# Kernel optimization log

Measured on AMD Instinct MI355X. Metric: run time of the kernel, lower is better.

## Reference

```python
import jax, jax.numpy as jnp
import numpy as np

NUM_HEADS = 32
NUM_KV_HEADS = 8
HEAD_DIM = 128
ROPE_THETA = 1000000.0
SCALING = HEAD_DIM ** -0.5


def apply_rope_neox(x, positions):
    # x: [T, H, D], positions: [T] int
    half = HEAD_DIM // 2
    inv_freq = 1.0 / (ROPE_THETA ** (jnp.arange(0, half, dtype=jnp.float32) / half))
    freqs = positions.astype(jnp.float32)[:, None] * inv_freq[None, :]  # [T, D/2]
    cos = jnp.cos(freqs)[:, None, :]  # [T, 1, D/2]
    sin = jnp.sin(freqs)[:, None, :]
    x1, x2 = x[..., :half], x[..., half:]
    return jnp.concatenate([x1 * cos - x2 * sin, x2 * cos + x1 * sin], axis=-1)


def setup_inputs() -> dict:
    key = jax.random.key(0)
    k1, k2, k3 = jax.random.split(key, 3)
    T, H = 2048, 4096
    positions = jnp.arange(T, dtype=jnp.int32)
    hidden_states = jax.random.normal(k1, (T, H), dtype=jnp.float32)
    Wqkv = jax.random.normal(k2, (H, 6144), dtype=jnp.float32) * 0.02
    Wo = jax.random.normal(k3, (H, H), dtype=jnp.float32) * 0.02
    return {"positions": positions, "hidden_states": hidden_states, "Wqkv": Wqkv, "Wo": Wo}


def reference(positions, hidden_states, Wqkv, Wo):
    T = hidden_states.shape[0]
    q_size = NUM_HEADS * HEAD_DIM
    kv_size = NUM_KV_HEADS * HEAD_DIM
    qkv = hidden_states @ Wqkv  # [T, 6144]
    q = qkv[:, :q_size].reshape(T, NUM_HEADS, HEAD_DIM)
    k = qkv[:, q_size:q_size + kv_size].reshape(T, NUM_KV_HEADS, HEAD_DIM)
    v = qkv[:, q_size + kv_size:].reshape(T, NUM_KV_HEADS, HEAD_DIM)
    q = apply_rope_neox(q, positions)
    k = apply_rope_neox(k, positions)
    # GQA: repeat kv heads to match query heads
    rep = NUM_HEADS // NUM_KV_HEADS
    k = jnp.repeat(k, rep, axis=1)  # [T, H, D]
    v = jnp.repeat(v, rep, axis=1)
    scores = jnp.einsum('thd,shd->hts', q, k) * SCALING  # [H, T, T]
    causal = jnp.tril(jnp.ones((T, T), dtype=bool))
    scores = jnp.where(causal[None], scores, jnp.finfo(scores.dtype).min)
    attn = jax.nn.softmax(scores, axis=-1)
    out = jnp.einsum('hts,shd->thd', attn, v).reshape(T, NUM_HEADS * HEAD_DIM)
    return out @ Wo
```

## Files before the change

### kernel.cpp

```cpp
#include <hip/hip_runtime.h>
#include <math.h>

#define T_TOK 2048
#define HDIM  4096
#define QKVN  6144
#define NHEADS 32
#define HD    128
#define KV_OFF 4096
#define V_OFF  5120
#define SCALE 0.08838834764831843f

typedef __attribute__((ext_vector_type(8))) short short8;
typedef __attribute__((ext_vector_type(4))) float f32x4;
typedef __attribute__((ext_vector_type(16))) float f32x16;

__device__ __forceinline__ ushort f2bf(float f) {
    union { float f; unsigned u; } v; v.f = f;
    unsigned r = v.u + 0x7FFFu + ((v.u >> 16) & 1u);
    return (ushort)(r >> 16);
}

template <int N_, int K_>
__global__ __launch_bounds__(256) void gemm_bf16(const ushort* __restrict__ A,
                                                 const ushort* __restrict__ B,
                                                 float* __restrict__ C) {
    __shared__ ushort As[128 * 32];
    __shared__ ushort Bs[128 * 32];

    const int tid = threadIdx.x;
    const int w = tid >> 6;
    const int l = tid & 63;
    const int bm = blockIdx.y * 128;
    const int bn = blockIdx.x * 128;
    const int wm = (w & 1) * 64;
    const int wn = (w >> 1) * 64;

    f32x4 acc[4][4];
#pragma unroll
    for (int i = 0; i < 4; i++)
#pragma unroll
        for (int j = 0; j < 4; j++) acc[i][j] = (f32x4){0.f, 0.f, 0.f, 0.f};

    const ushort* ag = A + (size_t)(bm + (tid >> 2)) * K_ + (tid & 3) * 8;
    const ushort* bg = B + (size_t)(bn + (tid >> 2)) * K_ + (tid & 3) * 8;

    auto ldsA = (__attribute__((address_space(3))) char*)As;
    auto ldsB = (__attribute__((address_space(3))) char*)Bs;
    const int wb = w * 1024;

    for (int k0 = 0; k0 < K_; k0 += 32) {
        __syncthreads();
        __builtin_amdgcn_global_load_lds(
            (const __attribute__((address_space(1))) void*)ag,
            (__attribute__((address_space(3))) void*)(ldsA + wb), 16, 0, 0);
        __builtin_amdgcn_global_load_lds(
            (const __attribute__((address_space(1))) void*)(ag + (size_t)64 * K_),
            (__attribute__((address_space(3))) void*)(ldsA + 4096 + wb), 16, 0, 0);
        __builtin_amdgcn_global_load_lds(
            (const __attribute__((address_space(1))) void*)bg,
            (__attribute__((address_space(3))) void*)(ldsB + wb), 16, 0, 0);
        __builtin_amdgcn_global_load_lds(
            (const __attribute__((address_space(1))) void*)(bg + (size_t)64 * K_),
            (__attribute__((address_space(3))) void*)(ldsB + 4096 + wb), 16, 0, 0);
        ag += 32;
        bg += 32;
        __syncthreads();

        short8 af[4], bfr[4];
#pragma unroll
        for (int i = 0; i < 4; i++)
            af[i] = *(const short8*)&As[(wm + 16 * i + (l & 15)) * 32 + (l >> 4) * 8];
#pragma unroll
        for (int j = 0; j < 4; j++)
            bfr[j] = *(const short8*)&Bs[(wn + 16 * j + (l & 15)) * 32 + (l >> 4) * 8];
#pragma unroll
        for (int i = 0; i < 4; i++)
#pragma unroll
            for (int j = 0; j < 4; j++)
                acc[i][j] = __builtin_amdgcn_mfma_f32_16x16x32_bf16(af[i], bfr[j], acc[i][j], 0, 0, 0);
    }

    const int cn = bn + wn + (l & 15);
    const int rm = bm + wm + (l >> 4) * 4;
#pragma unroll
    for (int i = 0; i < 4; i++)
#pragma unroll
        for (int j = 0; j < 4; j++)
#pragma unroll
            for (int r = 0; r < 4; r++)
                C[(size_t)(rm + 16 * i + r) * N_ + cn + 16 * j] = acc[i][j][r];
}

__global__ __launch_bounds__(256) void cast_bf16(const float* __restrict__ in,
                                                 ushort* __restrict__ outp) {
    const int i = (blockIdx.x * 256 + threadIdx.x) * 4;
    float4 v = *(const float4*)(in + i);
    ushort4 o = {f2bf(v.x), f2bf(v.y), f2bf(v.z), f2bf(v.w)};
    *(ushort4*)(outp + i) = o;
}

template <int K_, int N_>
__global__ __launch_bounds__(256) void transpose_cast(const float* __restrict__ W,
                                                      ushort* __restrict__ WT) {
    __shared__ float T[32 * 65];
    const int k0 = blockIdx.y * 32;
    const int n0 = blockIdx.x * 64;
    const int x = threadIdx.x & 63;
    const int y = threadIdx.x >> 6;
#pragma unroll
    for (int p = 0; p < 8; p++) {
        const int kk = p * 4 + y;
        T[kk * 65 + x] = W[(size_t)(k0 + kk) * N_ + n0 + x];
    }
    __syncthreads();
#pragma unroll
    for (int q = 0; q < 4; q++) {
        const int nl = q * 16 + (threadIdx.x >> 4);
        const int k2 = (threadIdx.x & 15) * 2;
        ushort2 o = {f2bf(T[k2 * 65 + nl]), f2bf(T[(k2 + 1) * 65 + nl])};
        *(ushort2*)&WT[(size_t)(n0 + nl) * K_ + k0 + k2] = o;
    }
}

__global__ __launch_bounds__(256) void rope_cast(const int* __restrict__ pos,
                                                 const float* __restrict__ qkv,
                                                 ushort* __restrict__ qkB) {
    const int t = blockIdx.x;
    const int slot = blockIdx.y * 4 + (threadIdx.x >> 6);
    const int d = threadIdx.x & 63;
    const float p = (float)pos[t];
    const float invf = exp2f(-(float)d * (19.931568569324174f / 64.0f));
    const float f = p * invf;
    const float c = cosf(f), s = sinf(f);
    const float sc = (slot < 32) ? SCALE : 1.0f;
    const float* base = qkv + (size_t)t * QKVN + slot * HD;
    ushort* ob = qkB + (size_t)t * QKVN + slot * HD;
    const float x1 = base[d];
    const float x2 = base[d + 64];
    ob[d]      = f2bf((x1 * c - x2 * s) * sc);
    ob[d + 64] = f2bf((x2 * c + x1 * s) * sc);
}

__global__ __launch_bounds__(256) void vt_cast(const float* __restrict__ qkv,
                                               ushort* __restrict__ Vt) {
    __shared__ float tile[32][33];
    const int t0 = blockIdx.x * 32;
    const int c0 = blockIdx.y * 32;
    const int tx = threadIdx.x & 31;
    const int ty = threadIdx.x >> 5;
#pragma unroll
    for (int i = 0; i < 4; i++) {
        const int tt = ty + 8 * i;
        tile[tt][tx] = qkv[(size_t)(t0 + tt) * QKVN + V_OFF + c0 + tx];
    }
    __syncthreads();
#pragma unroll
    for (int i = 0; i < 4; i++) {
        const int dd = ty + 8 * i;
        Vt[(size_t)(c0 + dd) * 2048 + t0 + tx] = f2bf(tile[tx][dd]);
    }
}

__global__ __launch_bounds__(256, 2) void flash_attn_mfma(
        const ushort* __restrict__ qkB,
        const ushort* __restrict__ Vt,
        ushort* __restrict__ attnB) {
    __shared__ ushort Kf[8 * 512];
    __shared__ ushort Vf[8 * 512];

    const int b = blockIdx.x;
    const int half = b >> 8;
    const int rest = b & 255;
    const int h = rest >> 3;
    const int q8 = rest & 7;
    const int qi = half ? (15 - q8) : q8;
    const int kvh = h >> 2;

    const int tid = threadIdx.x;
    const int w = tid >> 6;
    const int l = tid & 63;
    const int l31 = l & 31;
    const int hf = l >> 5;

    const int qg = qi * 128 + w * 32 + l31;

    short8 qf[8];
    {
        const ushort* qrow = qkB + (size_t)qg * QKVN + h * HD + hf * 8;
#pragma unroll
        for (int kt = 0; kt < 8; kt++)
            qf[kt] = *(const short8*)(qrow + kt * 16);
    }

    f32x16 O[4];
#pragma unroll
    for (int dt = 0; dt < 4; dt++)
#pragma unroll
        for (int r = 0; r < 16; r++) O[dt][r] = 0.f;
    float mcur = -INFINITY, lcur = 0.f;

    const ushort* kbase = qkB + (size_t)l31 * QKVN + KV_OFF + kvh * HD + (2 * w) * 16 + hf * 8;
    const ushort* vbase = Vt + ((size_t)(kvh * 128 + w * 32 + l31)) * 2048 + hf * 8;

    auto ldsK = (__attribute__((address_space(3))) char*)Kf;
    auto ldsV = (__attribute__((address_space(3))) char*)Vf;

    const int nst = 4 * qi + 4;
    const int mylast = 4 * qi + w;

    for (int st = 0; st < nst; st++) {
        __syncthreads();
        {
            const ushort* kg = kbase + (size_t)st * 32 * QKVN;
            __builtin_amdgcn_global_load_lds(
                (const __attribute__((address_space(1))) void*)kg,
                (__attribute__((address_space(3))) void*)(ldsK + (2 * w) * 1024), 16, 0, 0);
            __builtin_amdgcn_global_load_lds(
                (const __attribute__((address_space(1))) void*)(kg + 16),
                (__attribute__((address_space(3))) void*)(ldsK + (2 * w + 1) * 1024), 16, 0, 0);
            const ushort* vg = vbase + st * 32;
            __builtin_amdgcn_global_load_lds(
                (const __attribute__((address_space(1))) void*)vg,
                (__attribute__((address_space(3))) void*)(ldsV + (2 * w) * 1024), 16, 0, 0);
            __builtin_amdgcn_global_load_lds(
                (const __attribute__((address_space(1))) void*)(vg + 16),
                (__attribute__((address_space(3))) void*)(ldsV + (2 * w + 1) * 1024), 16, 0, 0);
        }
        __syncthreads();

        if (st <= mylast) {
            f32x16 S;
#pragma unroll
            for (int r = 0; r < 16; r++) S[r] = 0.f;
#pragma unroll
            for (int kt = 0; kt < 8; kt++) {
                short8 afK = *(const short8*)&Kf[kt * 512 + l * 8];
                S = __builtin_amdgcn_mfma_f32_32x32x16_bf16(afK, qf[kt], S, 0, 0, 0);
            }

            float p[16];
#pragma unroll
            for (int r = 0; r < 16; r++) p[r] = S[r];
            if (st == mylast) {
                const int sb = st * 32 + 4 * hf;
#pragma unroll
                for (int r = 0; r < 16; r++) {
                    const int sg = sb + (r & 3) + 8 * (r >> 2);
                    if (sg > qg) p[r] = -INFINITY;
                }
            }
            float rmax = p[0];
#pragma unroll
            for (int r = 1; r < 16; r++) rmax = fmaxf(rmax, p[r]);
            rmax = fmaxf(rmax, __shfl_xor(rmax, 32));
            const float mnew = fmaxf(mcur, rmax);
            const float alpha = __expf(mcur - mnew);
            float rsum = 0.f;
#pragma unroll
            for (int r = 0; r < 16; r++) {
                p[r] = __expf(p[r] - mnew);
                rsum += p[r];
            }
            rsum += __shfl_xor(rsum, 32);
            lcur = lcur * alpha + rsum;
            mcur = mnew;

#pragma unroll
            for (int dt = 0; dt < 4; dt++)
#pragma unroll
                for (int r = 0; r < 16; r++) O[dt][r] *= alpha;

            unsigned pk[8], rk[8];
#pragma unroll
            for (int g = 0; g < 4; g++) {
                pk[2 * g]     = (unsigned)f2bf(p[4 * g])     | ((unsigned)f2bf(p[4 * g + 1]) << 16);
                pk[2 * g + 1] = (unsigned)f2bf(p[4 * g + 2]) | ((unsigned)f2bf(p[4 * g + 3]) << 16);
            }
#pragma unroll
            for (int i = 0; i < 8; i++) rk[i] = (unsigned)__shfl_xor((int)pk[i], 32);

            short8 Pf[2];
#pragma unroll
            for (int kt2 = 0; kt2 < 2; kt2++) {
                const int g = 2 * kt2 + hf;
                union { unsigned u[4]; short8 s; } cvt;
                cvt.u[0] = hf ? rk[2 * g]     : pk[2 * g];
                cvt.u[1] = hf ? rk[2 * g + 1] : pk[2 * g + 1];
                cvt.u[2] = hf ? pk[2 * g]     : rk[2 * g];
                cvt.u[3] = hf ? pk[2 * g + 1] : rk[2 * g + 1];
                Pf[kt2] = cvt.s;
            }

#pragma unroll
            for (int dt = 0; dt < 4; dt++)
#pragma unroll
                for (int kt2 = 0; kt2 < 2; kt2++) {
                    short8 afV = *(const short8*)&Vf[(dt * 2 + kt2) * 512 + l * 8];
                    O[dt] = __builtin_amdgcn_mfma_f32_32x32x16_bf16(afV, Pf[kt2], O[dt], 0, 0, 0);
                }
        }
    }

    const float inv = 1.0f / lcur;
    ushort* orow = attnB + (size_t)qg * HDIM + h * HD + 4 * hf;
#pragma unroll
    for (int dt = 0; dt < 4; dt++)
#pragma unroll
        for (int rg = 0; rg < 4; rg++) {
            ushort4 o;
            o.x = f2bf(O[dt][4 * rg + 0] * inv);
            o.y = f2bf(O[dt][4 * rg + 1] * inv);
            o.z = f2bf(O[dt][4 * rg + 2] * inv);
            o.w = f2bf(O[dt][4 * rg + 3] * inv);
            *(ushort4*)(orow + dt * 32 + 8 * rg) = o;
        }
}

__global__ __launch_bounds__(256) void rope_kernel(const int* __restrict__ pos,
                                                   float* __restrict__ qkv) {
    const int t = blockIdx.x;
    const int head = blockIdx.y * 4 + (threadIdx.x >> 6);
    const int d = threadIdx.x & 63;
    const float p = (float)pos[t];
    const float invf = exp2f(-(float)d * (19.931568569324174f / 64.0f));
    const float f = p * invf;
    const float c = cosf(f), s = sinf(f);
    float* base = qkv + (size_t)t * QKVN + head * HD;
    const float x1 = base[d];
    const float x2 = base[d + 64];
    base[d]      = x1 * c - x2 * s;
    base[d + 64] = x2 * c + x1 * s;
}

#define DOT4(acc, a, b) acc += (a).x*(b).x + (a).y*(b).y + (a).z*(b).z + (a).w*(b).w
#define FMA4(o, p, v) { (o).x += (p)*(v).x; (o).y += (p)*(v).y; (o).z += (p)*(v).z; (o).w += (p)*(v).w; }

__global__ __launch_bounds__(256, 2) void flash_attn_f32(const float* __restrict__ qkv,
                                                         float* __restrict__ out) {
    __shared__ float Qs[64 * 132];
    __shared__ float KVs[32 * 132];
    __shared__ float Ps[64 * 34];
    const int b = blockIdx.x;
    const int half = (b >> 9) & 1;
    const int rest = b & 511;
    const int h = rest >> 4;
    const int qlo = rest & 15;
    const int qi = half ? (31 - qlo) : qlo;
    const int kvh = h >> 2;
    const int tid = threadIdx.x;
    const int tx = tid & 7;
    const int ty = tid >> 3;
    {
        const float* qbase = qkv + (size_t)(qi * 64) * QKVN + h * HD;
#pragma unroll
        for (int r = 0; r < 8; r++) {
            int idx = r * 256 + tid;
            int qrow = idx >> 5;
            int d = (idx & 31) * 4;
            float4 v = *(const float4*)(qbase + (size_t)qrow * QKVN + d);
            v.x *= SCALE; v.y *= SCALE; v.z *= SCALE; v.w *= SCALE;
            *(float4*)(Qs + qrow * 132 + d) = v;
        }
    }
    float m[2], lsm[2];
    float4 O[2][4];
#pragma unroll
    for (int i = 0; i < 2; i++) {
        m[i] = -INFINITY; lsm[i] = 0.f;
#pragma unroll
        for (int jj = 0; jj < 4; jj++) O[i][jj] = make_float4(0.f, 0.f, 0.f, 0.f);
    }
    const float* kbase = qkv + KV_OFF + kvh * HD;
    const float* vbase = qkv + V_OFF + kvh * HD;
    const int qg0 = qi * 64 + ty;
    const int nst = 2 * qi + 2;
    for (int st = 0; st < nst; st++) {
        __syncthreads();
#pragma unroll
        for (int r = 0; r < 4; r++) {
            int idx = r * 256 + tid;
            int srow = idx >> 5;
            int d = (idx & 31) * 4;
            *(float4*)(KVs + srow * 132 + d) =
                *(const float4*)(kbase + (size_t)(st * 32 + srow) * QKVN + d);
        }
        __syncthreads();
        float S[2][4];
#pragma unroll
        for (int i = 0; i < 2; i++)
#pragma unroll
            for (int j = 0; j < 4; j++) S[i][j] = 0.f;
#pragma unroll 4
        for (int kk = 0; kk < HD; kk += 4) {
            float4 q0 = *(const float4*)(Qs + ty * 132 + kk);
            float4 q1 = *(const float4*)(Qs + (ty + 32) * 132 + kk);
            float4 k0 = *(const float4*)(KVs + tx * 132 + kk);
            float4 k1 = *(const float4*)(KVs + (tx + 8) * 132 + kk);
            float4 k2 = *(const float4*)(KVs + (tx + 16) * 132 + kk);
            float4 k3 = *(const float4*)(KVs + (tx + 24) * 132 + kk);
            DOT4(S[0][0], q0, k0); DOT4(S[0][1], q0, k1);
            DOT4(S[0][2], q0, k2); DOT4(S[0][3], q0, k3);
            DOT4(S[1][0], q1, k0); DOT4(S[1][1], q1, k1);
            DOT4(S[1][2], q1, k2); DOT4(S[1][3], q1, k3);
        }
        const int sg0 = st * 32 + tx;
        float alpha[2];
#pragma unroll
        for (int i = 0; i < 2; i++) {
            const int qg = qg0 + 32 * i;
            float rmax = -INFINITY;
#pragma unroll
            for (int j = 0; j < 4; j++) {
                if (sg0 + 8 * j > qg) S[i][j] = -INFINITY;
                rmax = fmaxf(rmax, S[i][j]);
            }
#pragma unroll
            for (int off = 1; off < 8; off <<= 1)
                rmax = fmaxf(rmax, __shfl_xor(rmax, off));
            const float mnew = fmaxf(m[i], rmax);
            alpha[i] = __expf(m[i] - mnew);
            float rsum = 0.f;
#pragma unroll
            for (int j = 0; j < 4; j++) {
                S[i][j] = __expf(S[i][j] - mnew);
                rsum += S[i][j];
            }
#pragma unroll
            for (int off = 1; off < 8; off <<= 1)
                rsum += __shfl_xor(rsum, off);
            lsm[i] = lsm[i] * alpha[i] + rsum;
            m[i] = mnew;
        }
#pragma unroll
        for (int i = 0; i < 2; i++)
#pragma unroll
            for (int j = 0; j < 4; j++)
                Ps[(ty + 32 * i) * 34 + tx + 8 * j] = S[i][j];
        __syncthreads();
#pragma unroll
        for (int r = 0; r < 4; r++) {
            int idx = r * 256 + tid;
            int srow = idx >> 5;
            int d = (idx & 31) * 4;
            *(float4*)(KVs + srow * 132 + d) =
                *(const float4*)(vbase + (size_t)(st * 32 + srow) * QKVN + d);
        }
        __syncthreads();
#pragma unroll
        for (int i = 0; i < 2; i++) {
            const float a = alpha[i];
#pragma unroll
            for (int jj = 0; jj < 4; jj++) {
                O[i][jj].x *= a; O[i][jj].y *= a; O[i][jj].z *= a; O[i][jj].w *= a;
            }
        }
#pragma unroll 4
        for (int s = 0; s < 32; s++) {
            float p0 = Ps[ty * 34 + s];
            float p1 = Ps[(ty + 32) * 34 + s];
            const float* vr = KVs + s * 132 + 4 * tx;
            float4 v0 = *(const float4*)(vr);
            float4 v1 = *(const float4*)(vr + 32);
            float4 v2 = *(const float4*)(vr + 64);
            float4 v3 = *(const float4*)(vr + 96);
            FMA4(O[0][0], p0, v0); FMA4(O[0][1], p0, v1);
            FMA4(O[0][2], p0, v2); FMA4(O[0][3], p0, v3);
            FMA4(O[1][0], p1, v0); FMA4(O[1][1], p1, v1);
            FMA4(O[1][2], p1, v2); FMA4(O[1][3], p1, v3);
        }
    }
#pragma unroll
    for (int i = 0; i < 2; i++) {
        const float inv = 1.0f / lsm[i];
        float* orow = out + (size_t)(qi * 64 + ty + 32 * i) * HDIM + h * HD + 4 * tx;
#pragma unroll
        for (int jj = 0; jj < 4; jj++) {
            float4 wv = O[i][jj];
            wv.x *= inv; wv.y *= inv; wv.z *= inv; wv.w *= inv;
            *(float4*)(orow + 32 * jj) = wv;
        }
    }
}

template <int N_, int K_>
__global__ __launch_bounds__(256) void sgemm(const float* __restrict__ A,
                                             const float* __restrict__ B,
                                             float* __restrict__ C) {
    __shared__ float As[8][128];
    __shared__ float Bs[8][128];
    const int tid = threadIdx.x;
    const int bm = blockIdx.y * 128;
    const int bn = blockIdx.x * 128;
    const int tx = tid & 15;
    const int ty = tid >> 4;
    const int lm = tid >> 1;
    const int lkq = (tid & 1) * 4;
    const int lr = tid >> 5;
    const int lnq = (tid & 31) * 4;
    float acc[8][8];
#pragma unroll
    for (int i = 0; i < 8; i++)
#pragma unroll
        for (int j = 0; j < 8; j++) acc[i][j] = 0.f;
    const float* Aptr = A + (size_t)(bm + lm) * K_ + lkq;
    const float* Bptr = B + (size_t)lr * N_ + bn + lnq;
    for (int k0 = 0; k0 < K_; k0 += 8) {
        float4 av = *(const float4*)Aptr;
        float4 bv = *(const float4*)Bptr;
        __syncthreads();
        As[lkq + 0][lm] = av.x;
        As[lkq + 1][lm] = av.y;
        As[lkq + 2][lm] = av.z;
        As[lkq + 3][lm] = av.w;
        *(float4*)&Bs[lr][lnq] = bv;
        __syncthreads();
        Aptr += 8;
        Bptr += (size_t)8 * N_;
#pragma unroll
        for (int kk = 0; kk < 8; kk++) {
            float4 a0 = *(const float4*)&As[kk][ty * 4];
            float4 a1 = *(const float4*)&As[kk][64 + ty * 4];
            float4 b0 = *(const float4*)&Bs[kk][tx * 4];
            float4 b1 = *(const float4*)&Bs[kk][64 + tx * 4];
            float a[8] = {a0.x, a0.y, a0.z, a0.w, a1.x, a1.y, a1.z, a1.w};
            float bb[8] = {b0.x, b0.y, b0.z, b0.w, b1.x, b1.y, b1.z, b1.w};
#pragma unroll
            for (int i = 0; i < 8; i++)
#pragma unroll
                for (int j = 0; j < 8; j++) acc[i][j] += a[i] * bb[j];
        }
    }
#pragma unroll
    for (int i = 0; i < 8; i++) {
        int row = bm + ((i < 4) ? (ty * 4 + i) : (64 + ty * 4 + i - 4));
        float4 c0 = {acc[i][0], acc[i][1], acc[i][2], acc[i][3]};
        float4 c1 = {acc[i][4], acc[i][5], acc[i][6], acc[i][7]};
        *(float4*)&C[(size_t)row * N_ + bn + tx * 4] = c0;
        *(float4*)&C[(size_t)row * N_ + bn + 64 + tx * 4] = c1;
    }
}

extern "C" void kernel_launch(void* const* d_in, const int* in_sizes, int n_in,
                              void* d_out, int out_size, void* d_ws, size_t ws_size,
                              hipStream_t stream) {
    const int*   positions = (const int*)d_in[0];
    const float* hidden    = (const float*)d_in[1];
    const float* Wqkv      = (const float*)d_in[2];
    const float* Wo        = (const float*)d_in[3];
    float* out = (float*)d_out;

    char* ws = (char*)d_ws;
    float*  qkv   = (float*)ws;
    ushort* attnB = (ushort*)ws;
    ushort* WqkvT = (ushort*)(ws + 50331648);
    ushort* WoT   = (ushort*)(ws + 100663296);
    ushort* hA    = (ushort*)(ws + 134217728);
    ushort* qkB   = (ushort*)(ws + 134217728);
    ushort* Vt    = (ushort*)(ws + 159383552);
    const size_t NEEDED = 163577856;

    if (ws_size >= NEEDED) {
        cast_bf16<<<dim3((T_TOK * HDIM) / 1024), 256, 0, stream>>>(hidden, hA);
        transpose_cast<HDIM, QKVN><<<dim3(QKVN / 64, HDIM / 32), 256, 0, stream>>>(Wqkv, WqkvT);
        transpose_cast<HDIM, HDIM><<<dim3(HDIM / 64, HDIM / 32), 256, 0, stream>>>(Wo, WoT);
        gemm_bf16<QKVN, HDIM><<<dim3(QKVN / 128, T_TOK / 128), 256, 0, stream>>>(hA, WqkvT, qkv);
        rope_cast<<<dim3(T_TOK, 10), 256, 0, stream>>>(positions, qkv, qkB);
        vt_cast<<<dim3(T_TOK / 32, 32), 256, 0, stream>>>(qkv, Vt);
        flash_attn_mfma<<<dim3(512), 256, 0, stream>>>(qkB, Vt, attnB);
        gemm_bf16<HDIM, HDIM><<<dim3(HDIM / 128, T_TOK / 128), 256, 0, stream>>>(attnB, WoT, out);
    } else {
        float* attn = qkv + (size_t)T_TOK * QKVN;
        sgemm<QKVN, HDIM><<<dim3(QKVN / 128, T_TOK / 128), 256, 0, stream>>>(hidden, Wqkv, qkv);
        rope_kernel<<<dim3(T_TOK, 10), 256, 0, stream>>>(positions, qkv);
        flash_attn_f32<<<dim3(1024), 256, 0, stream>>>(qkv, attn);
        sgemm<HDIM, HDIM><<<dim3(HDIM / 128, T_TOK / 128), 256, 0, stream>>>(attn, Wo, out);
    }
}
```

Measured before the change: 691.9 us.

## Replace bf16 GEMM with 256x256-tile, 8-wave, double-buffered phased pipeline

Replaces the simple 128x128 bf16 GEMM with a 256x256 tile kernel using 512 threads, K-step 64, and double-buffered LDS fed by async global-to-LDS loads. Loads for future K-steps are interleaved with four MFMA phases separated by barriers and setprio. It also adds XOR swizzling of LDS columns to avoid bank conflicts and a workgroup-index swizzle for L2 locality. The goal is to hide global load latency and raise MFMA utilisation in both projection GEMMs. The cost is heavy LDS use (128KB) and many registers, which limits occupancy, and only 192 or 128 workgroups are launched.

```diff
diff --git a/kernel.cpp b/kernel.cpp
--- a/kernel.cpp
+++ b/kernel.cpp
@@ -21,74 +21,160 @@
 }
 
 template <int N_, int K_>
-__global__ __launch_bounds__(256) void gemm_bf16(const ushort* __restrict__ A,
-                                                 const ushort* __restrict__ B,
-                                                 float* __restrict__ C) {
-    __shared__ ushort As[128 * 32];
-    __shared__ ushort Bs[128 * 32];
-
-    const int tid = threadIdx.x;
+__global__ __launch_bounds__(512, 2) void gemm_bf16_8ph(const ushort* __restrict__ A,
+                                                        const ushort* __restrict__ B,
+                                                        float* __restrict__ C) {
+    __shared__ __attribute__((aligned(16))) ushort As[2][2][8192];
+    __shared__ __attribute__((aligned(16))) ushort Bs[2][2][8192];
+
+    constexpr int NT = K_ / 64;
+    constexpr int NBN = N_ / 256;
+
+    const int nwg = (int)gridDim.x;
+    const int bid = (int)blockIdx.x;
+    const int swz = (nwg & 7) ? bid : ((bid & 7) * (nwg >> 3) + (bid >> 3));
+    const int bm = (swz / NBN) * 256;
+    const int bn = (swz % NBN) * 256;
+
+    const int tid = (int)threadIdx.x;
     const int w = tid >> 6;
     const int l = tid & 63;
-    const int bm = blockIdx.y * 128;
-    const int bn = blockIdx.x * 128;
-    const int wm = (w & 1) * 64;
-    const int wn = (w >> 1) * 64;
-
-    f32x4 acc[4][4];
-#pragma unroll
-    for (int i = 0; i < 4; i++)
+    const int hfa = w >> 2;
+    const int hfb = (w & 3) >> 1;
+    const int wbr64 = (w & 1) * 4096;
+
+    const int arc = (l & 15) * 64;
+    const int ac0 = ((((l >> 4) << 4)) ^ ((l & 7) << 4)) >> 1;
+    const int ac1 = (((1 << 6) | ((l >> 4) << 4)) ^ ((l & 7) << 4)) >> 1;
+
+    const int grow = w * 8 + (l >> 3);
+    const int gcol = ((l & 7) ^ (l >> 3)) * 8;
+    const ushort* Ag = A + (size_t)(bm + grow) * K_ + gcol;
+    const ushort* Bg = B + (size_t)(bn + grow) * K_ + gcol;
+
+    auto ldsA = (__attribute__((address_space(3))) char*)&As[0][0][0];
+    auto ldsB = (__attribute__((address_space(3))) char*)&Bs[0][0][0];
+    const int wsl = w * 1024;
+
+#define STG2(ldsbase, gsrc, bufi, hfi, kt)                                                              \
+    do {                                                                                                \
+        __builtin_amdgcn_global_load_lds(                                                               \
+            (const __attribute__((address_space(1))) void*)((gsrc) + (size_t)((hfi) * 128) * K_ + (kt) * 64),       \
+            (__attribute__((address_space(3))) void*)((ldsbase) + (bufi) * 32768 + (hfi) * 16384 + wsl), 16, 0, 0);  \
+        __builtin_amdgcn_global_load_lds(                                                               \
+            (const __attribute__((address_space(1))) void*)((gsrc) + (size_t)((hfi) * 128 + 64) * K_ + (kt) * 64),  \
+            (__attribute__((address_space(3))) void*)((ldsbase) + (bufi) * 32768 + (hfi) * 16384 + 8192 + wsl), 16, 0, 0); \
+    } while (0)
+
+    STG2(ldsB, Bg, 0, 0, 0);
+    STG2(ldsB, Bg, 0, 1, 0);
+    STG2(ldsA, Ag, 0, 0, 0);
+    STG2(ldsA, Ag, 0, 1, 0);
+    STG2(ldsB, Bg, 1, 0, 1);
+    STG2(ldsB, Bg, 1, 1, 1);
+    STG2(ldsA, Ag, 1, 0, 1);
+    asm volatile("s_waitcnt vmcnt(6)" ::: "memory");
+    __builtin_amdgcn_s_barrier();
+
+    f32x4 acc[8][4];
+#pragma unroll
+    for (int i = 0; i < 8; i++)
 #pragma unroll
         for (int j = 0; j < 4; j++) acc[i][j] = (f32x4){0.f, 0.f, 0.f, 0.f};
 
-    const ushort* ag = A + (size_t)(bm + (tid >> 2)) * K_ + (tid & 3) * 8;
-    const ushort* bg = B + (size_t)(bn + (tid >> 2)) * K_ + (tid & 3) * 8;
-
-    auto ldsA = (__attribute__((address_space(3))) char*)As;
-    auto ldsB = (__attribute__((address_space(3))) char*)Bs;
-    const int wb = w * 1024;
-
-    for (int k0 = 0; k0 < K_; k0 += 32) {
-        __syncthreads();
-        __builtin_amdgcn_global_load_lds(
-            (const __attribute__((address_space(1))) void*)ag,
-            (__attribute__((address_space(3))) void*)(ldsA + wb), 16, 0, 0);
-        __builtin_amdgcn_global_load_lds(
-            (const __attribute__((address_space(1))) void*)(ag + (size_t)64 * K_),
-            (__attribute__((address_space(3))) void*)(ldsA + 4096 + wb), 16, 0, 0);
-        __builtin_amdgcn_global_load_lds(
-            (const __attribute__((address_space(1))) void*)bg,
-            (__attribute__((address_space(3))) void*)(ldsB + wb), 16, 0, 0);
-        __builtin_amdgcn_global_load_lds(
-            (const __attribute__((address_space(1))) void*)(bg + (size_t)64 * K_),
-            (__attribute__((address_space(3))) void*)(ldsB + 4096 + wb), 16, 0, 0);
-        ag += 32;
-        bg += 32;
-        __syncthreads();
-
-        short8 af[4], bfr[4];
-#pragma unroll
-        for (int i = 0; i < 4; i++)
-            af[i] = *(const short8*)&As[(wm + 16 * i + (l & 15)) * 32 + (l >> 4) * 8];
-#pragma unroll
-        for (int j = 0; j < 4; j++)
-            bfr[j] = *(const short8*)&Bs[(wn + 16 * j + (l & 15)) * 32 + (l >> 4) * 8];
-#pragma unroll
-        for (int i = 0; i < 4; i++)
-#pragma unroll
-            for (int j = 0; j < 4; j++)
-                acc[i][j] = __builtin_amdgcn_mfma_f32_16x16x32_bf16(af[i], bfr[j], acc[i][j], 0, 0, 0);
-    }
-
-    const int cn = bn + wn + (l & 15);
-    const int rm = bm + wm + (l >> 4) * 4;
-#pragma unroll
-    for (int i = 0; i < 4; i++)
-#pragma unroll
-        for (int j = 0; j < 4; j++)
+    short8 a0[4][2], a1[4][2], bq[4][2];
+
+    int buf = 0;
+    for (int t = 0; t < NT; ++t) {
+        const int nb = buf ^ 1;
+        const ushort* Abuf = &As[buf][hfa][0];
+        const ushort* Bbuf = &Bs[buf][hfb][0] + wbr64;
+
+#pragma unroll
+        for (int fi = 0; fi < 4; fi++) {
+            a0[fi][0] = *(const short8*)(Abuf + fi * 1024 + arc + ac0);
+            a0[fi][1] = *(const short8*)(Abuf + fi * 1024 + arc + ac1);
+        }
+#pragma unroll
+        for (int fj = 0; fj < 4; fj++) {
+            bq[fj][0] = *(const short8*)(Bbuf + fj * 1024 + arc + ac0);
+            bq[fj][1] = *(const short8*)(Bbuf + fj * 1024 + arc + ac1);
+        }
+        if (t + 1 < NT) STG2(ldsA, Ag, nb, 1, t + 1);
+        __builtin_amdgcn_s_barrier();
+        __builtin_amdgcn_s_setprio(1);
+#pragma unroll
+        for (int fi = 0; fi < 4; fi++)
+#pragma unroll
+            for (int fj = 0; fj < 2; fj++)
+#pragma unroll
+                for (int s = 0; s < 2; s++)
+                    acc[fi][fj] = __builtin_amdgcn_mfma_f32_16x16x32_bf16(a0[fi][s], bq[fj][s], acc[fi][fj], 0, 0, 0);
+        __builtin_amdgcn_s_setprio(0);
+        __builtin_amdgcn_s_barrier();
+
+        if (t + 2 < NT) STG2(ldsB, Bg, buf, 0, t + 2);
+        __builtin_amdgcn_s_barrier();
+        __builtin_amdgcn_s_setprio(1);
+#pragma unroll
+        for (int fi = 0; fi < 4; fi++)
+#pragma unroll
+            for (int fj = 2; fj < 4; fj++)
+#pragma unroll
+                for (int s = 0; s < 2; s++)
+                    acc[fi][fj] = __builtin_amdgcn_mfma_f32_16x16x32_bf16(a0[fi][s], bq[fj][s], acc[fi][fj], 0, 0, 0);
+        __builtin_amdgcn_s_setprio(0);
+        __builtin_amdgcn_s_barrier();
+
+#pragma unroll
+        for (int fi = 0; fi < 4; fi++) {
+            a1[fi][0] = *(const short8*)(Abuf + (fi + 4) * 1024 + arc + ac0);
+            a1[fi][1] = *(const short8*)(Abuf + (fi + 4) * 1024 + arc + ac1);
+        }
+        if (t + 2 < NT) STG2(ldsB, Bg, buf, 1, t + 2);
+        __builtin_amdgcn_s_barrier();
+        __builtin_amdgcn_s_setprio(1);
+#pragma unroll
+        for (int fi = 0; fi < 4; fi++)
+#pragma unroll
+            for (int fj = 2; fj < 4; fj++)
+#pragma unroll
+                for (int s = 0; s < 2; s++)
+                    acc[fi + 4][fj] = __builtin_amdgcn_mfma_f32_16x16x32_bf16(a1[fi][s], bq[fj][s], acc[fi + 4][fj], 0, 0, 0);
+        __builtin_amdgcn_s_setprio(0);
+        __builtin_amdgcn_s_barrier();
+
+        if (t + 2 < NT) {
+            STG2(ldsA, Ag, buf, 0, t + 2);
+            asm volatile("s_waitcnt vmcnt(6)" ::: "memory");
+        } else {
+            asm volatile("s_waitcnt vmcnt(0)" ::: "memory");
+        }
+        __builtin_amdgcn_s_barrier();
+        __builtin_amdgcn_s_setprio(1);
+#pragma unroll
+        for (int fi = 0; fi < 4; fi++)
+#pragma unroll
+            for (int fj = 0; fj < 2; fj++)
+#pragma unroll
+                for (int s = 0; s < 2; s++)
+                    acc[fi + 4][fj] = __builtin_amdgcn_mfma_f32_16x16x32_bf16(a1[fi][s], bq[fj][s], acc[fi + 4][fj], 0, 0, 0);
+        __builtin_amdgcn_s_setprio(0);
+        __builtin_amdgcn_s_barrier();
+
+        buf = nb;
+    }
+#undef STG2
+
+    const int cn = bn + (w & 3) * 64 + (l & 15);
+    const int rm = bm + hfa * 128 + ((l >> 4) << 2);
+#pragma unroll
+    for (int fi = 0; fi < 8; fi++)
+#pragma unroll
+        for (int fj = 0; fj < 4; fj++)
 #pragma unroll
             for (int r = 0; r < 4; r++)
-                C[(size_t)(rm + 16 * i + r) * N_ + cn + 16 * j] = acc[i][j][r];
+                C[(size_t)(rm + 16 * fi + r) * N_ + cn + 16 * fj] = acc[fi][fj][r];
 }
 
 __global__ __launch_bounds__(256) void cast_bf16(const float* __restrict__ in,
@@ -563,11 +649,11 @@
         cast_bf16<<<dim3((T_TOK * HDIM) / 1024), 256, 0, stream>>>(hidden, hA);
         transpose_cast<HDIM, QKVN><<<dim3(QKVN / 64, HDIM / 32), 256, 0, stream>>>(Wqkv, WqkvT);
         transpose_cast<HDIM, HDIM><<<dim3(HDIM / 64, HDIM / 32), 256, 0, stream>>>(Wo, WoT);
-        gemm_bf16<QKVN, HDIM><<<dim3(QKVN / 128, T_TOK / 128), 256, 0, stream>>>(hA, WqkvT, qkv);
+        gemm_bf16_8ph<QKVN, HDIM><<<dim3((T_TOK / 256) * (QKVN / 256)), 512, 0, stream>>>(hA, WqkvT, qkv);
         rope_cast<<<dim3(T_TOK, 10), 256, 0, stream>>>(positions, qkv, qkB);
         vt_cast<<<dim3(T_TOK / 32, 32), 256, 0, stream>>>(qkv, Vt);
         flash_attn_mfma<<<dim3(512), 256, 0, stream>>>(qkB, Vt, attnB);
-        gemm_bf16<HDIM, HDIM><<<dim3(HDIM / 128, T_TOK / 128), 256, 0, stream>>>(attnB, WoT, out);
+        gemm_bf16_8ph<HDIM, HDIM><<<dim3((T_TOK / 256) * (HDIM / 256)), 512, 0, stream>>>(attnB, WoT, out);
     } else {
         float* attn = qkv + (size_t)T_TOK * QKVN;
         sgemm<QKVN, HDIM><<<dim3(QKVN / 128, T_TOK / 128), 256, 0, stream>>>(hidden, Wqkv, qkv);
```

New measurement: 671.9 us. -2.9%, faster.
